# Kernel tuning notes

Hardware: AMD Instinct MI355X
Metric: run time of the kernel (lower is better)

Reference implementation:

```python
import jax, jax.numpy as jnp
import numpy as np
from jax import lax

I, H, O, T = 256, 1024, 1, 16384

def setup_inputs() -> dict:
    key = jax.random.key(0)
    ks = jax.random.split(key, 10)
    k = 1.0 / np.sqrt(H)
    u = lambda kk, shp, lim: jax.random.uniform(kk, shp, jnp.float32, -lim, lim)
    return {
        "input_seq": jax.random.normal(ks[0], (1, T, I), jnp.float32),
        # LSTM params (PyTorch layout: [4H, in], gate order i,f,g,o)
        "W_ih": u(ks[1], (4 * H, I), k),
        "W_hh": u(ks[2], (4 * H, H), k),
        "b_ih": u(ks[3], (4 * H,), k),
        "b_hh": u(ks[4], (4 * H,), k),
        # MLP head: Linear(H,H) -> ReLU -> Linear(H,O)
        "W1": u(ks[5], (H, H), k),
        "b1": u(ks[6], (H,), k),
        "W2": u(ks[7], (O, H), k),
        "b2": u(ks[8], (O,), k),
    }

def reference(input_seq, W_ih, W_hh, b_ih, b_hh, W1, b1, W2, b2):
    x = input_seq[0]                       # [T, I] (batch must be 1, see forward's h.reshape(1,-1))
    # Precompute input contribution to gates for all timesteps in one GEMM.
    xg = x @ W_ih.T + (b_ih + b_hh)        # [T, 4H]

    def step(carry, xg_t):
        h, c = carry                       # [H], [H]
        g = xg_t + h @ W_hh.T              # [4H]
        i, f, gg, o = jnp.split(g, 4)
        i = jax.nn.sigmoid(i)
        f = jax.nn.sigmoid(f)
        gg = jnp.tanh(gg)
        o = jax.nn.sigmoid(o)
        c = f * c + i * gg
        h = o * jnp.tanh(c)
        return (h, c), None

    h0 = jnp.zeros((H,), dtype=x.dtype)
    c0 = jnp.zeros((H,), dtype=x.dtype)
    (h, c), _ = lax.scan(step, (h0, c0), xg)

    hflat = h[None, :]                     # h.reshape(1, -1) with B=1 -> [1, H]
    z = jax.nn.relu(hflat @ W1.T + b1)     # [1, H]
    return z @ W2.T + b2                   # [1, O]
```

## Files before the change

kernel.cpp:

```cpp
#include <hip/hip_runtime.h>
#include <cstdint>

#define I_DIM   256
#define H_DIM   1024
#define T_STEPS 16384
#define NBLK    128
#define CELLS   8
#define ROWS    32
#define THREADS 512

__launch_bounds__(THREADS, 2)
__global__ void lstm_persist(const float* __restrict__ x,
                             const float* __restrict__ W_ih,
                             const float* __restrict__ W_hh,
                             const float* __restrict__ b_ih,
                             const float* __restrict__ b_hh,
                             unsigned long long* __restrict__ ring)
{
    __shared__ __align__(16) float h_cur[H_DIM];
    __shared__ __align__(16) float xbuf[2][I_DIM];
    __shared__ float grow[ROWS];

    const int tid = threadIdx.x;
    const int blk = blockIdx.x;
    const int r   = tid >> 4;
    const int l   = tid & 15;
    const int q   = r >> 3;
    const int m   = r & 7;
    const int row_g = q * H_DIM + blk * CELLS + m;

    float w[64];
    {
        const float4* Wrow = reinterpret_cast<const float4*>(W_hh + (size_t)row_g * H_DIM);
        #pragma unroll
        for (int jj = 0; jj < 16; ++jj)
            *reinterpret_cast<float4*>(&w[jj * 4]) = Wrow[jj * 16 + l];
    }
    float wih[16];
    {
        const float4* Wrow = reinterpret_cast<const float4*>(W_ih + (size_t)row_g * I_DIM);
        #pragma unroll
        for (int s = 0; s < 4; ++s)
            *reinterpret_cast<float4*>(&wih[s * 4]) = Wrow[l * 4 + s];
    }
    const float bias_r = b_ih[row_g] + b_hh[row_g];

    if (tid < 64)
        *reinterpret_cast<float4*>(&xbuf[0][tid * 4]) =
            *reinterpret_cast<const float4*>(x + tid * 4);
    __syncthreads();

    float xg = (l == 0) ? bias_r : 0.f;
    #pragma unroll
    for (int kk = 0; kk < 16; ++kk) xg += wih[kk] * xbuf[0][l * 16 + kk];

    if (tid < 64)
        *reinterpret_cast<float4*>(&xbuf[1][tid * 4]) =
            *reinterpret_cast<const float4*>(x + I_DIM + tid * 4);
    int   cur     = 1;
    float c_state = 0.f;

    for (int t = 0; t < T_STEPS; ++t) {
        float4 xpre;
        if (tid < 64) {
            const int tt = (t + 2 < T_STEPS) ? t + 2 : T_STEPS - 1;
            xpre = *reinterpret_cast<const float4*>(x + (size_t)tt * I_DIM + tid * 4);
        }
        float2 hv;
        if (t == 0) {
            hv.x = 0.f; hv.y = 0.f;
        } else {
            const unsigned long long want = (unsigned long long)(t - 1);
            unsigned long long* p = ring + (((t - 1) & 1) ? H_DIM : 0) + 2 * tid;
            unsigned long long v0 = 0, v1 = 0;
            bool g0 = false, g1 = false;
            do {
                if (!g0) { v0 = __hip_atomic_load(p,     __ATOMIC_RELAXED, __HIP_MEMORY_SCOPE_AGENT); g0 = ((v0 >> 32) == want); }
                if (!g1) { v1 = __hip_atomic_load(p + 1, __ATOMIC_RELAXED, __HIP_MEMORY_SCOPE_AGENT); g1 = ((v1 >> 32) == want); }
            } while (!(g0 && g1));
            hv.x = __uint_as_float((unsigned)v0);
            hv.y = __uint_as_float((unsigned)v1);
        }
        *reinterpret_cast<float2*>(&h_cur[2 * tid]) = hv;
        __syncthreads();

        float acc = xg;
        #pragma unroll
        for (int jj = 0; jj < 16; ++jj) {
            const float4 h4 = *reinterpret_cast<const float4*>(&h_cur[jj * 64 + l * 4]);
            acc += w[jj * 4 + 0] * h4.x + w[jj * 4 + 1] * h4.y +
                   w[jj * 4 + 2] * h4.z + w[jj * 4 + 3] * h4.w;
        }
        acc += __shfl_xor(acc, 1);
        acc += __shfl_xor(acc, 2);
        acc += __shfl_xor(acc, 4);
        acc += __shfl_xor(acc, 8);
        if (l == 0) grow[r] = acc;
        __syncthreads();

        if (tid < CELLS) {
            float gi = grow[tid];
            float gf = grow[8 + tid];
            float gg = grow[16 + tid];
            float go = grow[24 + tid];
            gi = 1.f / (1.f + expf(-gi));
            gf = 1.f / (1.f + expf(-gf));
            gg = tanhf(gg);
            go = 1.f / (1.f + expf(-go));
            c_state = gf * c_state + gi * gg;
            const float h_new = go * tanhf(c_state);
            const unsigned long long pack =
                ((unsigned long long)t << 32) | (unsigned long long)__float_as_uint(h_new);
            __hip_atomic_store(ring + ((t & 1) ? H_DIM : 0) + blk * CELLS + tid, pack,
                               __ATOMIC_RELAXED, __HIP_MEMORY_SCOPE_AGENT);
        }

        float xg_n = (l == 0) ? bias_r : 0.f;
        #pragma unroll
        for (int kk = 0; kk < 16; ++kk) xg_n += wih[kk] * xbuf[cur][l * 16 + kk];
        xg = xg_n;
        if (tid < 64)
            *reinterpret_cast<float4*>(&xbuf[cur ^ 1][tid * 4]) = xpre;
        cur ^= 1;
    }
}

__global__ void ffn_kernel(const unsigned long long* __restrict__ ring,
                           const float* __restrict__ W1,
                           const float* __restrict__ b1,
                           const float* __restrict__ W2,
                           float* __restrict__ partials)
{
    __shared__ float psum[8];
    const int tid = threadIdx.x;
    const int r2  = tid >> 5;
    const int l2  = tid & 31;
    const int j   = blockIdx.x * 8 + r2;
    const unsigned long long* hslot = ring + (((T_STEPS - 1) & 1) ? H_DIM : 0);

    float acc = 0.f;
    #pragma unroll 8
    for (int kk = 0; kk < 32; ++kk) {
        const int   k  = kk * 32 + l2;
        const float hk = __uint_as_float((unsigned)hslot[k]);
        acc += hk * W1[(size_t)j * H_DIM + k];
    }
    acc += __shfl_xor(acc, 1);
    acc += __shfl_xor(acc, 2);
    acc += __shfl_xor(acc, 4);
    acc += __shfl_xor(acc, 8);
    acc += __shfl_xor(acc, 16);
    if (l2 == 0) {
        float z = acc + b1[j];
        z = z > 0.f ? z : 0.f;
        psum[r2] = z * W2[j];
    }
    __syncthreads();
    if (tid == 0) {
        float s = 0.f;
        #pragma unroll
        for (int i = 0; i < 8; ++i) s += psum[i];
        partials[blockIdx.x] = s;
    }
}

__global__ void out_kernel(const float* __restrict__ partials,
                           const float* __restrict__ b2,
                           float* __restrict__ out)
{
    __shared__ float ws2[2];
    const int tid = threadIdx.x;
    float v = partials[tid];
    v += __shfl_xor(v, 1);
    v += __shfl_xor(v, 2);
    v += __shfl_xor(v, 4);
    v += __shfl_xor(v, 8);
    v += __shfl_xor(v, 16);
    v += __shfl_xor(v, 32);
    if ((tid & 63) == 0) ws2[tid >> 6] = v;
    __syncthreads();
    if (tid == 0) out[0] = ws2[0] + ws2[1] + b2[0];
}

extern "C" void kernel_launch(void* const* d_in, const int* in_sizes, int n_in,
                              void* d_out, int out_size, void* d_ws, size_t ws_size,
                              hipStream_t stream)
{
    const float* x    = (const float*)d_in[0];
    const float* W_ih = (const float*)d_in[1];
    const float* W_hh = (const float*)d_in[2];
    const float* b_ih = (const float*)d_in[3];
    const float* b_hh = (const float*)d_in[4];
    const float* W1   = (const float*)d_in[5];
    const float* b1   = (const float*)d_in[6];
    const float* W2   = (const float*)d_in[7];
    const float* b2   = (const float*)d_in[8];
    float* out = (float*)d_out;

    unsigned long long* ring = (unsigned long long*)d_ws;
    const size_t ring_bytes = (size_t)2 * H_DIM * sizeof(unsigned long long);
    float* partials = (float*)((char*)d_ws + ring_bytes);

    hipMemsetAsync(d_ws, 0xAA, ring_bytes, stream);

    lstm_persist<<<NBLK, THREADS, 0, stream>>>(x, W_ih, W_hh, b_ih, b_hh, ring);
    ffn_kernel<<<128, 256, 0, stream>>>(ring, W1, b1, W2, partials);
    out_kernel<<<1, 128, 0, stream>>>(partials, b2, out);
}
```

Before: 35.14 ms.

## Map each cell's four gates into one wavefront to drop shared-memory gate barrier

Remaps threads so each 64-lane wavefront owns one LSTM cell, with its four 16-lane groups computing the i/f/g/o gate rows. Gate values are exchanged by wavefront shuffles instead of a shared-memory array, which removes one __syncthreads and the serial tid<8 gate tail on each timestep's critical path. The W_ih slice is also re-indexed so the input projection reads float4 from LDS without bank conflicts. Every lane now evaluates the transcendentals redundantly, and a barrier is moved to protect the xbuf double buffer.

```diff
diff --git a/kernel.cpp b/kernel.cpp
--- a/kernel.cpp
+++ b/kernel.cpp
@@ -6,7 +6,6 @@
 #define T_STEPS 16384
 #define NBLK    128
 #define CELLS   8
-#define ROWS    32
 #define THREADS 512
 
 __launch_bounds__(THREADS, 2)
@@ -19,29 +18,25 @@
 {
     __shared__ __align__(16) float h_cur[H_DIM];
     __shared__ __align__(16) float xbuf[2][I_DIM];
-    __shared__ float grow[ROWS];
 
     const int tid = threadIdx.x;
     const int blk = blockIdx.x;
-    const int r   = tid >> 4;
+    const int wv  = tid >> 6;
+    const int q   = (tid >> 4) & 3;
     const int l   = tid & 15;
-    const int q   = r >> 3;
-    const int m   = r & 7;
-    const int row_g = q * H_DIM + blk * CELLS + m;
-
-    float w[64];
+    const int row_g = q * H_DIM + blk * CELLS + wv;
+
+    float4 w4[16];
     {
         const float4* Wrow = reinterpret_cast<const float4*>(W_hh + (size_t)row_g * H_DIM);
         #pragma unroll
-        for (int jj = 0; jj < 16; ++jj)
-            *reinterpret_cast<float4*>(&w[jj * 4]) = Wrow[jj * 16 + l];
-    }
-    float wih[16];
+        for (int jj = 0; jj < 16; ++jj) w4[jj] = Wrow[jj * 16 + l];
+    }
+    float4 wih4[4];
     {
         const float4* Wrow = reinterpret_cast<const float4*>(W_ih + (size_t)row_g * I_DIM);
         #pragma unroll
-        for (int s = 0; s < 4; ++s)
-            *reinterpret_cast<float4*>(&wih[s * 4]) = Wrow[l * 4 + s];
+        for (int s = 0; s < 4; ++s) wih4[s] = Wrow[s * 16 + l];
     }
     const float bias_r = b_ih[row_g] + b_hh[row_g];
 
@@ -52,7 +47,10 @@
 
     float xg = (l == 0) ? bias_r : 0.f;
     #pragma unroll
-    for (int kk = 0; kk < 16; ++kk) xg += wih[kk] * xbuf[0][l * 16 + kk];
+    for (int s = 0; s < 4; ++s) {
+        const float4 xv = *reinterpret_cast<const float4*>(&xbuf[0][s * 64 + l * 4]);
+        xg += wih4[s].x * xv.x + wih4[s].y * xv.y + wih4[s].z * xv.z + wih4[s].w * xv.w;
+    }
 
     if (tid < 64)
         *reinterpret_cast<float4*>(&xbuf[1][tid * 4]) =
@@ -88,37 +86,37 @@
         #pragma unroll
         for (int jj = 0; jj < 16; ++jj) {
             const float4 h4 = *reinterpret_cast<const float4*>(&h_cur[jj * 64 + l * 4]);
-            acc += w[jj * 4 + 0] * h4.x + w[jj * 4 + 1] * h4.y +
-                   w[jj * 4 + 2] * h4.z + w[jj * 4 + 3] * h4.w;
+            acc += w4[jj].x * h4.x + w4[jj].y * h4.y + w4[jj].z * h4.z + w4[jj].w * h4.w;
         }
         acc += __shfl_xor(acc, 1);
         acc += __shfl_xor(acc, 2);
         acc += __shfl_xor(acc, 4);
         acc += __shfl_xor(acc, 8);
-        if (l == 0) grow[r] = acc;
-        __syncthreads();
-
-        if (tid < CELLS) {
-            float gi = grow[tid];
-            float gf = grow[8 + tid];
-            float gg = grow[16 + tid];
-            float go = grow[24 + tid];
-            gi = 1.f / (1.f + expf(-gi));
-            gf = 1.f / (1.f + expf(-gf));
-            gg = tanhf(gg);
-            go = 1.f / (1.f + expf(-go));
-            c_state = gf * c_state + gi * gg;
-            const float h_new = go * tanhf(c_state);
+        const float gi_r = __shfl(acc, 0);
+        const float gf_r = __shfl(acc, 16);
+        const float gg_r = __shfl(acc, 32);
+        const float go_r = __shfl(acc, 48);
+        const float gi = 1.f / (1.f + expf(-gi_r));
+        const float gf = 1.f / (1.f + expf(-gf_r));
+        const float gg = tanhf(gg_r);
+        const float go = 1.f / (1.f + expf(-go_r));
+        c_state = gf * c_state + gi * gg;
+        const float h_new = go * tanhf(c_state);
+        if ((tid & 63) == 0) {
             const unsigned long long pack =
                 ((unsigned long long)t << 32) | (unsigned long long)__float_as_uint(h_new);
-            __hip_atomic_store(ring + ((t & 1) ? H_DIM : 0) + blk * CELLS + tid, pack,
+            __hip_atomic_store(ring + ((t & 1) ? H_DIM : 0) + blk * CELLS + wv, pack,
                                __ATOMIC_RELAXED, __HIP_MEMORY_SCOPE_AGENT);
         }
 
         float xg_n = (l == 0) ? bias_r : 0.f;
         #pragma unroll
-        for (int kk = 0; kk < 16; ++kk) xg_n += wih[kk] * xbuf[cur][l * 16 + kk];
+        for (int s = 0; s < 4; ++s) {
+            const float4 xv = *reinterpret_cast<const float4*>(&xbuf[cur][s * 64 + l * 4]);
+            xg_n += wih4[s].x * xv.x + wih4[s].y * xv.y + wih4[s].z * xv.z + wih4[s].w * xv.w;
+        }
         xg = xg_n;
+        __syncthreads();
         if (tid < 64)
             *reinterpret_cast<float4*>(&xbuf[cur ^ 1][tid * 4]) = xpre;
         cur ^= 1;
```

Result: no change. 34.52 ms (-1.8%).
